# Kernel tuning notes

Measured on AMD Instinct MI355X. Metric: run time of the kernel, lower is better.

Reference implementation:

```python
import jax, jax.numpy as jnp
import numpy as np

B, LH, HF = 65536, 128, 32
VC_MIN = 0.0


def _theta_init():
    # Deterministic parameter init, matching the torch constructor defaults.
    def spinv(x):
        return float(np.log(np.exp(max(x, 1e-4)) - 1.0 + 1e-6))
    vals = [
        0.0,                                  # alpha_raw: log(0.5/(1-0.5))
        float(np.log(np.exp(1.0) - 1.0 + 1e-6)),   # c_raw  (c_init=1.0)
        float(np.log(np.exp(0.1) - 1.0 + 1e-6)),   # kappa_raw (kappa_init=0.1)
        float(np.log(np.exp(0.15) - 1.0 + 1e-6)),  # vc_raw (vc_eff=0.15)
        -6.0,   # log_qx
        -6.0,   # log_qu
        -5.0,   # log_r
        0.0,    # log_q_scale
        -6.0,   # log_p0_xx
        -4.0,   # log_p0_uu
        spinv(0.1),   # a1_raw
        spinv(0.05),  # d1_raw
        spinv(0.5),   # d2_raw
        spinv(0.5),   # d3_raw
        0.0,    # b1
        0.0,    # b2
        0.1,    # beta
        float(np.arctanh(0.9)),  # rho_m_raw
        -4.0,   # log_qm
        -4.0,   # log_p0_mm
    ]
    return np.asarray(vals, dtype=np.float32)


def setup_inputs() -> dict:
    key = jax.random.key(0)
    k1, k2, k3, k4, k5 = jax.random.split(key, 5)
    return {
        "v_hist": jax.random.normal(k1, (B, LH), dtype=jnp.float32),
        "dt_hist": 0.01 + 0.1 * jax.random.uniform(k2, (B, LH), dtype=jnp.float32),
        "x_obs_hist": jax.random.normal(k3, (B, LH), dtype=jnp.float32),
        "v_fut": jax.random.normal(k4, (B, HF), dtype=jnp.float32),
        "dt_fut": 0.01 + 0.1 * jax.random.uniform(k5, (B, HF), dtype=jnp.float32),
        "theta": jnp.asarray(_theta_init()),
    }


def _forward(v_hist, dt_hist, x_obs_hist, v_fut, dt_fut, theta):
    sp = jax.nn.softplus
    alpha = jax.nn.sigmoid(theta[0])
    c = sp(theta[1]); kappa = sp(theta[2]); vc = sp(theta[3]) + VC_MIN
    qx = jnp.exp(theta[4]); qu = jnp.exp(theta[5]); R = jnp.exp(theta[6])
    qs = jnp.exp(theta[7]); p0xx = jnp.exp(theta[8]); p0uu = jnp.exp(theta[9])
    a1 = sp(theta[10]); d1 = sp(theta[11]); d2 = sp(theta[12]); d3 = sp(theta[13])
    b1 = theta[14]; b2 = theta[15]; beta = theta[16]
    rho_m = jnp.tanh(theta[17]); qm = jnp.exp(theta[18]); p0mm = jnp.exp(theta[19])

    Bn, Lh = v_hist.shape
    dtype = v_hist.dtype
    eye = jnp.eye(3, dtype=dtype)

    def predict(s, P, v, dv, dt):
        x, u, m = s[:, 0], s[:, 1], s[:, 2]
        rho = jnp.exp(-alpha * dt)
        forcing = jax.nn.relu(v * v - vc * vc)
        cl = (-a1 * u + b1 * v + b2 * dv
              - d1 * u * u - d2 * u * jnp.abs(v) - d3 * u * jnp.abs(u))
        x_p = x + u * dt
        u_p = rho * u - kappa * x * dt + c * forcing * dt + cl * dt + beta * m
        m_p = rho_m * m
        s_p = jnp.stack([x_p, u_p, m_p], axis=1)
        z = jnp.zeros_like(dt); o = jnp.ones_like(dt)
        Fm = jnp.stack([
            jnp.stack([o, dt, z], axis=1),
            jnp.stack([-kappa * dt, rho, beta * o], axis=1),
            jnp.stack([z, z, rho_m * o], axis=1)], axis=1)  # [B,3,3]
        qdiag = jnp.stack([qs * qx * dt, qs * qu * dt, qm * o], axis=1)  # [B,3]
        P_p = jnp.einsum('bij,bjk,blk->bil', Fm, P, Fm) + qdiag[:, :, None] * eye
        return s_p, P_p

    def update(s, P, y):
        innov = y - s[:, 0]
        S = P[:, 0, 0] + R
        K = P[:, :, 0] / S[:, None]            # [B,3]
        s_u = s + K * innov[:, None]
        IKH = eye - K[:, :, None] * eye[0]     # I - K H, H = [1,0,0]
        P_u = (jnp.einsum('bij,bjk,blk->bil', IKH, P, IKH)
               + R * (K[:, :, None] * K[:, None, :]))
        return s_u, P_u

    s0 = jnp.zeros((Bn, 3), dtype).at[:, 0].set(x_obs_hist[:, 0])
    P0 = jnp.broadcast_to(jnp.diag(jnp.stack([p0xx, p0uu, p0mm])).astype(dtype),
                          (Bn, 3, 3))

    # History steps k = 1 .. Lh-1 (scan over time axis, [T, B] layout)
    v_h = v_hist[:, :Lh - 1].T
    dv_h = jnp.concatenate(
        [jnp.zeros((1, Bn), dtype), (v_hist[:, 1:Lh - 1] - v_hist[:, :Lh - 2]).T], axis=0)
    dt_h = jnp.maximum(dt_hist[:, 1:], 1e-6).T
    y_h = x_obs_hist[:, 1:].T

    def hist_step(carry, inp):
        s, P = carry
        v, dv, dt, y = inp
        s, P = predict(s, P, v, dv, dt)
        s, P = update(s, P, y)
        return (s, P), None

    (s, P), _ = jax.lax.scan(hist_step, (s0, P0), (v_h, dv_h, dt_h, y_h))

    # Future rollout (predict only)
    v_f = v_fut.T
    dv_f = (v_fut - jnp.concatenate([v_hist[:, -1:], v_fut[:, :-1]], axis=1)).T
    dt_f = jnp.maximum(dt_fut, 1e-6).T

    def fut_step(carry, inp):
        s, P = carry
        v, dv, dt = inp
        s, P = predict(s, P, v, dv, dt)
        return (s, P), (s[:, 0], P[:, 0, 0], s[:, 1])

    _, (x_preds, x_vars, u_ests) = jax.lax.scan(fut_step, (s, P), (v_f, dv_f, dt_f))
    return x_preds.T, x_vars.T, u_ests.T  # each [B, Hf]


def reference(v_hist, dt_hist, x_obs_hist, v_fut, dt_fut, theta):
    return _forward(v_hist, dt_hist, x_obs_hist, v_fut, dt_fut, theta)
```

## Files before the change

kernel.cpp:

```cpp
#include <hip/hip_runtime.h>
#include <math.h>

#define BATCH 65536
#define LHIST 128
#define HFUT  32

__device__ __forceinline__ float softplusf(float x) {
    return fmaxf(x, 0.0f) + log1pf(expf(-fabsf(x)));
}

__global__ __launch_bounds__(256, 1) void kalman_fwd(
    const float* __restrict__ v_hist,
    const float* __restrict__ dt_hist,
    const float* __restrict__ x_obs,
    const float* __restrict__ v_fut,
    const float* __restrict__ dt_fut,
    const float* __restrict__ theta,
    float* __restrict__ out)
{
    const int b = blockIdx.x * blockDim.x + threadIdx.x;

    const float alpha = 1.0f / (1.0f + expf(-theta[0]));
    const float c     = softplusf(theta[1]);
    const float kappa = softplusf(theta[2]);
    const float vc    = softplusf(theta[3]);
    const float qx    = expf(theta[4]);
    const float qu    = expf(theta[5]);
    const float Rn    = expf(theta[6]);
    const float qs    = expf(theta[7]);
    const float p0xx  = expf(theta[8]);
    const float p0uu  = expf(theta[9]);
    const float a1    = softplusf(theta[10]);
    const float d1    = softplusf(theta[11]);
    const float d2    = softplusf(theta[12]);
    const float d3    = softplusf(theta[13]);
    const float b1    = theta[14];
    const float b2    = theta[15];
    const float beta  = theta[16];
    const float rho_m = tanhf(theta[17]);
    const float qm    = expf(theta[18]);
    const float p0mm  = expf(theta[19]);
    const float vc2   = vc * vc;
    const float qxs   = qs * qx;
    const float qus   = qs * qu;
    const float rm2   = rho_m * rho_m;
    const float nal2e = -alpha * 1.44269504088896340736f;

    float sx = 0.0f, su = 0.0f, sm = 0.0f;
    float p00 = p0xx, p01 = 0.0f, p02 = 0.0f, p11 = p0uu, p12 = 0.0f, p22 = p0mm;

    auto predict = [&](float v, float dv, float dt_raw) {
        float dt  = fmaxf(dt_raw, 1e-6f);
        float rho = __builtin_amdgcn_exp2f(nal2e * dt);
        float forcing = fmaxf(v * v - vc2, 0.0f);
        float cl = -a1 * su + b1 * v + b2 * dv
                 - d1 * su * su - d2 * su * fabsf(v) - d3 * su * fabsf(su);
        float kdt = kappa * dt;
        float x_p = sx + su * dt;
        float u_p = rho * su - kdt * sx + c * forcing * dt + cl * dt + beta * sm;
        float m_p = rho_m * sm;
        float f0 = p00 + dt * p01;
        float f1 = p01 + dt * p11;
        float f2 = p02 + dt * p12;
        float g0 = -kdt * p00 + rho * p01 + beta * p02;
        float g1 = -kdt * p01 + rho * p11 + beta * p12;
        float g2 = -kdt * p02 + rho * p12 + beta * p22;
        float n00 = f0 + dt * f1 + qxs * dt;
        float n01 = -kdt * f0 + rho * f1 + beta * f2;
        float n02 = rho_m * f2;
        float n11 = -kdt * g0 + rho * g1 + beta * g2 + qus * dt;
        float n12 = rho_m * g2;
        float n22 = rm2 * p22 + qm;
        sx = x_p; su = u_p; sm = m_p;
        p00 = n00; p01 = n01; p02 = n02; p11 = n11; p12 = n12; p22 = n22;
    };

    auto update = [&](float y) {
        float innov = y - sx;
        float S    = p00 + Rn;
        float Sinv = __builtin_amdgcn_rcpf(S);
        float K0 = p00 * Sinv, K1 = p01 * Sinv, K2 = p02 * Sinv;
        sx += K0 * innov; su += K1 * innov; sm += K2 * innov;
        float a = 1.0f - K0;
        float n00 = a * a * p00 + Rn * K0 * K0;
        float n01 = a * (p01 - K1 * p00) + Rn * K0 * K1;
        float n02 = a * (p02 - K2 * p00) + Rn * K0 * K2;
        float n11 = S * K1 * K1 - 2.0f * K1 * p01 + p11;
        float n12 = S * K1 * K2 - K2 * p01 - K1 * p02 + p12;
        float n22 = S * K2 * K2 - 2.0f * K2 * p02 + p22;
        p00 = n00; p01 = n01; p02 = n02; p11 = n11; p12 = n12; p22 = n22;
    };

    const float4* v4 = (const float4*)(v_hist  + (size_t)b * LHIST);
    const float4* d4 = (const float4*)(dt_hist + (size_t)b * LHIST);
    const float4* y4 = (const float4*)(x_obs   + (size_t)b * LHIST);

    float vp1, vp2;

    float4 cvv = v4[0], cdd = d4[0], cyy = y4[0];
    float4 pv  = v4[1], pd  = d4[1], py  = y4[1];
    {
        const float* vv = (const float*)&cvv;
        const float* dd = (const float*)&cdd;
        const float* yy = (const float*)&cyy;
        sx = yy[0]; vp1 = vv[0]; vp2 = vv[0];
        #pragma unroll
        for (int m = 1; m < 4; ++m) {
            float vcur = vv[m];
            predict(vp1, vp1 - vp2, dd[m]);
            update(yy[m]);
            vp2 = vp1; vp1 = vcur;
        }
    }

    #pragma unroll 1
    for (int g = 1; g < LHIST / 4; ++g) {
        cvv = pv; cdd = pd; cyy = py;
        int gn = (g < LHIST / 4 - 1) ? g + 1 : g;
        pv = v4[gn]; pd = d4[gn]; py = y4[gn];
        const float* vv = (const float*)&cvv;
        const float* dd = (const float*)&cdd;
        const float* yy = (const float*)&cyy;
        #pragma unroll
        for (int m = 0; m < 4; ++m) {
            float vcur = vv[m];
            predict(vp1, vp1 - vp2, dd[m]);
            update(yy[m]);
            vp2 = vp1; vp1 = vcur;
        }
    }

    const float4* vf4 = (const float4*)(v_fut  + (size_t)b * HFUT);
    const float4* df4 = (const float4*)(dt_fut + (size_t)b * HFUT);
    float4* xp = (float4*)(out + (size_t)b * HFUT);
    float4* xv = (float4*)(out + (size_t)BATCH * HFUT + (size_t)b * HFUT);
    float4* ue = (float4*)(out + 2 * (size_t)BATCH * HFUT + (size_t)b * HFUT);

    float vp = vp1;
    float4 fv = vf4[0], fd = df4[0];
    float4 qv = vf4[1], qd = df4[1];
    #pragma unroll 1
    for (int g = 0; g < HFUT / 4; ++g) {
        const float* vv = (const float*)&fv;
        const float* dd = (const float*)&fd;
        float4 ox, ov, ou;
        float* oxp = (float*)&ox; float* ovp = (float*)&ov; float* oup = (float*)&ou;
        #pragma unroll
        for (int m = 0; m < 4; ++m) {
            predict(vv[m], vv[m] - vp, dd[m]);
            vp = vv[m];
            oxp[m] = sx; ovp[m] = p00; oup[m] = su;
        }
        xp[g] = ox; xv[g] = ov; ue[g] = ou;
        fv = qv; fd = qd;
        int gn = (g < HFUT / 4 - 2) ? g + 2 : HFUT / 4 - 1;
        qv = vf4[gn]; qd = df4[gn];
    }
}

extern "C" void kernel_launch(void* const* d_in, const int* in_sizes, int n_in,
                              void* d_out, int out_size, void* d_ws, size_t ws_size,
                              hipStream_t stream) {
    const float* v_hist  = (const float*)d_in[0];
    const float* dt_hist = (const float*)d_in[1];
    const float* x_obs   = (const float*)d_in[2];
    const float* v_fut   = (const float*)d_in[3];
    const float* dt_fut  = (const float*)d_in[4];
    const float* theta   = (const float*)d_in[5];
    float* out = (float*)d_out;

    dim3 grid(BATCH / 256), block(256);
    hipLaunchKernelGGL(kalman_fwd, grid, block, 0, stream,
                       v_hist, dt_hist, x_obs, v_fut, dt_fut, theta, out);
}
```

Before: 200.7 us.

## Split Kalman covariance and state recursions into pipelined warp groups via LDS

Each block now has 512 threads. The first 256 threads run the covariance recursion and compute the Kalman gains, which do not depend on the state. They write the gains into a double-buffered shared-memory array, one 16-step chunk at a time. The other 256 threads read those gains one chunk later and run only the state recursion, with a barrier between chunks. The goal is to shorten the serial dependency chain per thread and overlap the two recursions, at the cost of 96KB of LDS per block, per-chunk syncs and duplicated dt loads.

```diff
diff --git a/kernel.cpp b/kernel.cpp
--- a/kernel.cpp
+++ b/kernel.cpp
@@ -9,7 +9,9 @@
     return fmaxf(x, 0.0f) + log1pf(expf(-fabsf(x)));
 }
 
-__global__ __launch_bounds__(256, 1) void kalman_fwd(
+#define KSLOT(buf, st, c, row) ((((((buf)*16 + (st))*3 + (c))*256)) + (row))
+
+__global__ __launch_bounds__(512, 2) void kalman_fwd(
     const float* __restrict__ v_hist,
     const float* __restrict__ dt_hist,
     const float* __restrict__ x_obs,
@@ -18,7 +20,12 @@
     const float* __restrict__ theta,
     float* __restrict__ out)
 {
-    const int b = blockIdx.x * blockDim.x + threadIdx.x;
+    const int tid = threadIdx.x;
+    const bool isP = (tid < 256);
+    const int row  = tid & 255;
+    const int b    = blockIdx.x * 256 + row;
+
+    __shared__ float Kls[2 * 16 * 3 * 256];
 
     const float alpha = 1.0f / (1.0f + expf(-theta[0]));
     const float c     = softplusf(theta[1]);
@@ -46,19 +53,13 @@
     const float rm2   = rho_m * rho_m;
     const float nal2e = -alpha * 1.44269504088896340736f;
 
-    float sx = 0.0f, su = 0.0f, sm = 0.0f;
     float p00 = p0xx, p01 = 0.0f, p02 = 0.0f, p11 = p0uu, p12 = 0.0f, p22 = p0mm;
-
-    auto predict = [&](float v, float dv, float dt_raw) {
+    float sx = 0.0f, su = 0.0f, sm = 0.0f, vp1 = 0.0f, vp2 = 0.0f;
+
+    auto P_step = [&](float dt_raw, int buf, int st) {
         float dt  = fmaxf(dt_raw, 1e-6f);
         float rho = __builtin_amdgcn_exp2f(nal2e * dt);
-        float forcing = fmaxf(v * v - vc2, 0.0f);
-        float cl = -a1 * su + b1 * v + b2 * dv
-                 - d1 * su * su - d2 * su * fabsf(v) - d3 * su * fabsf(su);
         float kdt = kappa * dt;
-        float x_p = sx + su * dt;
-        float u_p = rho * su - kdt * sx + c * forcing * dt + cl * dt + beta * sm;
-        float m_p = rho_m * sm;
         float f0 = p00 + dt * p01;
         float f1 = p01 + dt * p11;
         float f2 = p02 + dt * p12;
@@ -71,90 +72,156 @@
         float n11 = -kdt * g0 + rho * g1 + beta * g2 + qus * dt;
         float n12 = rho_m * g2;
         float n22 = rm2 * p22 + qm;
+        float S    = n00 + Rn;
+        float Sinv = __builtin_amdgcn_rcpf(S);
+        float K0 = n00 * Sinv, K1 = n01 * Sinv, K2 = n02 * Sinv;
+        Kls[KSLOT(buf, st, 0, row)] = K0;
+        Kls[KSLOT(buf, st, 1, row)] = K1;
+        Kls[KSLOT(buf, st, 2, row)] = K2;
+        float a = 1.0f - K0;
+        p00 = a * a * n00 + Rn * K0 * K0;
+        p01 = a * (n01 - K1 * n00) + Rn * K0 * K1;
+        p02 = a * (n02 - K2 * n00) + Rn * K0 * K2;
+        p11 = S * K1 * K1 - 2.0f * K1 * n01 + n11;
+        p12 = S * K1 * K2 - K2 * n01 - K1 * n02 + n12;
+        p22 = S * K2 * K2 - 2.0f * K2 * n02 + n22;
+    };
+
+    auto P_pred = [&](float dt_raw) {
+        float dt  = fmaxf(dt_raw, 1e-6f);
+        float rho = __builtin_amdgcn_exp2f(nal2e * dt);
+        float kdt = kappa * dt;
+        float f0 = p00 + dt * p01;
+        float f1 = p01 + dt * p11;
+        float f2 = p02 + dt * p12;
+        float g0 = -kdt * p00 + rho * p01 + beta * p02;
+        float g1 = -kdt * p01 + rho * p11 + beta * p12;
+        float g2 = -kdt * p02 + rho * p12 + beta * p22;
+        float n00 = f0 + dt * f1 + qxs * dt;
+        float n01 = -kdt * f0 + rho * f1 + beta * f2;
+        float n02 = rho_m * f2;
+        float n11 = -kdt * g0 + rho * g1 + beta * g2 + qus * dt;
+        float n12 = rho_m * g2;
+        float n22 = rm2 * p22 + qm;
+        p00 = n00; p01 = n01; p02 = n02; p11 = n11; p12 = n12; p22 = n22;
+    };
+
+    auto s_pred = [&](float v, float dv, float dt_raw) {
+        float dt  = fmaxf(dt_raw, 1e-6f);
+        float rho = __builtin_amdgcn_exp2f(nal2e * dt);
+        float forcing = fmaxf(v * v - vc2, 0.0f);
+        float cl = -a1 * su + b1 * v + b2 * dv
+                 - d1 * su * su - d2 * su * fabsf(v) - d3 * su * fabsf(su);
+        float kdt = kappa * dt;
+        float x_p = sx + su * dt;
+        float u_p = rho * su - kdt * sx + c * forcing * dt + cl * dt + beta * sm;
+        float m_p = rho_m * sm;
         sx = x_p; su = u_p; sm = m_p;
-        p00 = n00; p01 = n01; p02 = n02; p11 = n11; p12 = n12; p22 = n22;
-    };
-
-    auto update = [&](float y) {
+    };
+
+    auto s_step = [&](float vnew, float dt_raw, float y, int buf, int st) {
+        float K0 = Kls[KSLOT(buf, st, 0, row)];
+        float K1 = Kls[KSLOT(buf, st, 1, row)];
+        float K2 = Kls[KSLOT(buf, st, 2, row)];
+        s_pred(vp1, vp1 - vp2, dt_raw);
         float innov = y - sx;
-        float S    = p00 + Rn;
-        float Sinv = __builtin_amdgcn_rcpf(S);
-        float K0 = p00 * Sinv, K1 = p01 * Sinv, K2 = p02 * Sinv;
         sx += K0 * innov; su += K1 * innov; sm += K2 * innov;
-        float a = 1.0f - K0;
-        float n00 = a * a * p00 + Rn * K0 * K0;
-        float n01 = a * (p01 - K1 * p00) + Rn * K0 * K1;
-        float n02 = a * (p02 - K2 * p00) + Rn * K0 * K2;
-        float n11 = S * K1 * K1 - 2.0f * K1 * p01 + p11;
-        float n12 = S * K1 * K2 - K2 * p01 - K1 * p02 + p12;
-        float n22 = S * K2 * K2 - 2.0f * K2 * p02 + p22;
-        p00 = n00; p01 = n01; p02 = n02; p11 = n11; p12 = n12; p22 = n22;
+        vp2 = vp1; vp1 = vnew;
     };
 
     const float4* v4 = (const float4*)(v_hist  + (size_t)b * LHIST);
     const float4* d4 = (const float4*)(dt_hist + (size_t)b * LHIST);
     const float4* y4 = (const float4*)(x_obs   + (size_t)b * LHIST);
 
-    float vp1, vp2;
-
-    float4 cvv = v4[0], cdd = d4[0], cyy = y4[0];
-    float4 pv  = v4[1], pd  = d4[1], py  = y4[1];
     {
-        const float* vv = (const float*)&cvv;
-        const float* dd = (const float*)&cdd;
-        const float* yy = (const float*)&cyy;
-        sx = yy[0]; vp1 = vv[0]; vp2 = vv[0];
-        #pragma unroll
-        for (int m = 1; m < 4; ++m) {
-            float vcur = vv[m];
-            predict(vp1, vp1 - vp2, dd[m]);
-            update(yy[m]);
-            vp2 = vp1; vp1 = vcur;
+        if (isP) {
+            float cdt[16];
+            float4* C = (float4*)cdt;
+            #pragma unroll
+            for (int i = 0; i < 4; ++i) C[i] = d4[i];
+            #pragma unroll
+            for (int st = 1; st < 16; ++st) P_step(cdt[st], 0, st);
+        }
+        __syncthreads();
+
+        #pragma unroll 1
+        for (int k = 1; k < 8; ++k) {
+            if (isP) {
+                float cdt[16];
+                float4* C = (float4*)cdt;
+                #pragma unroll
+                for (int i = 0; i < 4; ++i) C[i] = d4[k * 4 + i];
+                int buf = k & 1;
+                P_step(cdt[0], buf, 0);
+                #pragma unroll
+                for (int st = 1; st < 16; ++st) P_step(cdt[st], buf, st);
+            } else {
+                int j = k - 1;
+                float cv[16], cd[16], cy[16];
+                float4* V = (float4*)cv; float4* D = (float4*)cd; float4* Y = (float4*)cy;
+                #pragma unroll
+                for (int i = 0; i < 4; ++i) {
+                    V[i] = v4[j * 4 + i]; D[i] = d4[j * 4 + i]; Y[i] = y4[j * 4 + i];
+                }
+                int buf = j & 1;
+                if (j == 0) {
+                    sx = cy[0]; vp1 = cv[0]; vp2 = cv[0];
+                } else {
+                    s_step(cv[0], cd[0], cy[0], buf, 0);
+                }
+                #pragma unroll
+                for (int st = 1; st < 16; ++st) s_step(cv[st], cd[st], cy[st], buf, st);
+            }
+            __syncthreads();
+        }
+
+        if (!isP) {
+            const int j = 7;
+            float cv[16], cd[16], cy[16];
+            float4* V = (float4*)cv; float4* D = (float4*)cd; float4* Y = (float4*)cy;
+            #pragma unroll
+            for (int i = 0; i < 4; ++i) {
+                V[i] = v4[j * 4 + i]; D[i] = d4[j * 4 + i]; Y[i] = y4[j * 4 + i];
+            }
+            s_step(cv[0], cd[0], cy[0], 1, 0);
+            #pragma unroll
+            for (int st = 1; st < 16; ++st) s_step(cv[st], cd[st], cy[st], 1, st);
         }
     }
 
-    #pragma unroll 1
-    for (int g = 1; g < LHIST / 4; ++g) {
-        cvv = pv; cdd = pd; cyy = py;
-        int gn = (g < LHIST / 4 - 1) ? g + 1 : g;
-        pv = v4[gn]; pd = d4[gn]; py = y4[gn];
-        const float* vv = (const float*)&cvv;
-        const float* dd = (const float*)&cdd;
-        const float* yy = (const float*)&cyy;
-        #pragma unroll
-        for (int m = 0; m < 4; ++m) {
-            float vcur = vv[m];
-            predict(vp1, vp1 - vp2, dd[m]);
-            update(yy[m]);
-            vp2 = vp1; vp1 = vcur;
-        }
-    }
-
-    const float4* vf4 = (const float4*)(v_fut  + (size_t)b * HFUT);
-    const float4* df4 = (const float4*)(dt_fut + (size_t)b * HFUT);
-    float4* xp = (float4*)(out + (size_t)b * HFUT);
-    float4* xv = (float4*)(out + (size_t)BATCH * HFUT + (size_t)b * HFUT);
-    float4* ue = (float4*)(out + 2 * (size_t)BATCH * HFUT + (size_t)b * HFUT);
-
-    float vp = vp1;
-    float4 fv = vf4[0], fd = df4[0];
-    float4 qv = vf4[1], qd = df4[1];
-    #pragma unroll 1
-    for (int g = 0; g < HFUT / 4; ++g) {
-        const float* vv = (const float*)&fv;
-        const float* dd = (const float*)&fd;
-        float4 ox, ov, ou;
-        float* oxp = (float*)&ox; float* ovp = (float*)&ov; float* oup = (float*)&ou;
-        #pragma unroll
-        for (int m = 0; m < 4; ++m) {
-            predict(vv[m], vv[m] - vp, dd[m]);
-            vp = vv[m];
-            oxp[m] = sx; ovp[m] = p00; oup[m] = su;
-        }
-        xp[g] = ox; xv[g] = ov; ue[g] = ou;
-        fv = qv; fd = qd;
-        int gn = (g < HFUT / 4 - 2) ? g + 2 : HFUT / 4 - 1;
-        qv = vf4[gn]; qd = df4[gn];
+    if (isP) {
+        float fdt[32];
+        float4* FD = (float4*)fdt;
+        const float4* df4 = (const float4*)(dt_fut + (size_t)b * HFUT);
+        #pragma unroll
+        for (int i = 0; i < 8; ++i) FD[i] = df4[i];
+        float oxv[32];
+        #pragma unroll
+        for (int j = 0; j < HFUT; ++j) { P_pred(fdt[j]); oxv[j] = p00; }
+        float4* xv = (float4*)(out + (size_t)BATCH * HFUT + (size_t)b * HFUT);
+        float4* OXV = (float4*)oxv;
+        #pragma unroll
+        for (int i = 0; i < 8; ++i) xv[i] = OXV[i];
+    } else {
+        float fv[32], fdt[32];
+        float4* FV = (float4*)fv; float4* FD = (float4*)fdt;
+        const float4* vf4 = (const float4*)(v_fut  + (size_t)b * HFUT);
+        const float4* df4 = (const float4*)(dt_fut + (size_t)b * HFUT);
+        #pragma unroll
+        for (int i = 0; i < 8; ++i) { FV[i] = vf4[i]; FD[i] = df4[i]; }
+        float oxp[32], oue[32];
+        float vp = vp1;
+        #pragma unroll
+        for (int j = 0; j < HFUT; ++j) {
+            s_pred(fv[j], fv[j] - vp, fdt[j]);
+            vp = fv[j];
+            oxp[j] = sx; oue[j] = su;
+        }
+        float4* xp = (float4*)(out + (size_t)b * HFUT);
+        float4* ue = (float4*)(out + 2 * (size_t)BATCH * HFUT + (size_t)b * HFUT);
+        float4* OXP = (float4*)oxp; float4* OUE = (float4*)oue;
+        #pragma unroll
+        for (int i = 0; i < 8; ++i) { xp[i] = OXP[i]; ue[i] = OUE[i]; }
     }
 }
 
@@ -169,7 +236,7 @@
     const float* theta   = (const float*)d_in[5];
     float* out = (float*)d_out;
 
-    dim3 grid(BATCH / 256), block(256);
+    dim3 grid(BATCH / 256), block(512);
     hipLaunchKernelGGL(kalman_fwd, grid, block, 0, stream,
                        v_hist, dt_hist, x_obs, v_fut, dt_fut, theta, out);
 }
```

Result: faster. 179.6 us (-10.5%).
